# Optimization experiments

Measured on AMD Instinct MI355X. Metric: run time of the kernel, lower is better.

## Reference

```python
import jax, jax.numpy as jnp
import numpy as np

B, S, D = 2, 2048, 2048
H = 16
DR = 64      # qk_rope_head_dim
DN = 64      # qk_nope_head_dim
DQK = DN + DR
DV = 128     # v_head_dim
QLR = 1536   # q_lora_rank
KVLR = 1024  # kv_lora_rank
THETA = 10000.0


def setup_inputs() -> dict:
    key = jax.random.key(0)
    ks = jax.random.split(key, 8)
    init = lambda k, shape: (jax.random.normal(k, shape, jnp.float32) * 0.02)
    x = jax.random.normal(ks[0], (B, S, D), jnp.float32)
    wq_a = init(ks[1], (QLR, D))
    q_norm_w = jnp.ones((QLR,), jnp.float32)
    wq_b = init(ks[2], (H * DQK, QLR))
    wkv_a = init(ks[3], (KVLR + DR, D))
    kv_norm_w = jnp.ones((KVLR,), jnp.float32)
    wkv_b = init(ks[4], (H * (DN + DV), KVLR))
    wo = init(ks[5], (D, H * DV))
    # rotary frequencies: angle[t, i] = t / theta^(2i/DR)  (complex freqs_cis = cos + i sin)
    inv_freq = 1.0 / (THETA ** (jnp.arange(0, DR, 2, dtype=jnp.float32) / DR))
    ang = jnp.arange(S, dtype=jnp.float32)[:, None] * inv_freq[None, :]  # [S, DR/2]
    freqs_cos, freqs_sin = jnp.cos(ang), jnp.sin(ang)
    # causal additive mask (large negative instead of -inf for grad safety)
    mask = jnp.where(jnp.triu(jnp.ones((S, S), bool), 1), -1e9, 0.0).astype(jnp.float32)
    return dict(x=x, wq_a=wq_a, q_norm_w=q_norm_w, wq_b=wq_b, wkv_a=wkv_a,
                kv_norm_w=kv_norm_w, wkv_b=wkv_b, wo=wo, mask=mask,
                freqs_cos=freqs_cos, freqs_sin=freqs_sin, start_pos=0)


def _rmsnorm(x, w, eps=1e-6):
    return x * jax.lax.rsqrt(jnp.mean(x * x, axis=-1, keepdims=True) + eps) * w


def _rope(x, cos, sin):
    # x: [B, S, h, d]; complex multiply on interleaved (even, odd) pairs
    x0, x1 = x[..., ::2], x[..., 1::2]
    c = cos[None, :, None, :]
    s = sin[None, :, None, :]
    return jnp.stack([x0 * c - x1 * s, x0 * s + x1 * c], axis=-1).reshape(x.shape)


def reference(x, wq_a, q_norm_w, wq_b, wkv_a, kv_norm_w, wkv_b, wo,
              mask, freqs_cos, freqs_sin, start_pos):
    # start_pos == 0 prefill: KV cache[:end_pos] equals current K/V.
    scale = DQK ** -0.5
    # low-rank Q: wq_b(q_norm(wq_a(x)))
    q = _rmsnorm(x @ wq_a.T, q_norm_w) @ wq_b.T
    q = q.reshape(B, S, H, DQK)
    q_nope, q_pe = q[..., :DN], q[..., DN:]
    q_pe = _rope(q_pe, freqs_cos, freqs_sin)
    # latent KV
    kv = x @ wkv_a.T                              # [B, S, KVLR + DR]
    c_kv, k_pe = kv[..., :KVLR], kv[..., KVLR:]
    k_pe = _rope(k_pe[:, :, None, :], freqs_cos, freqs_sin)   # [B, S, 1, DR]
    kv2 = (_rmsnorm(c_kv, kv_norm_w) @ wkv_b.T).reshape(B, S, H, DN + DV)
    k_nope, v = kv2[..., :DN], kv2[..., DN:]
    k = jnp.concatenate([k_nope, jnp.broadcast_to(k_pe, (B, S, H, DR))], axis=-1)
    qf = jnp.concatenate([q_nope, q_pe], axis=-1)             # [B, S, H, DQK]
    # scores laid out [B, S(q), H, T(k)] as in the torch code
    scores = jnp.einsum('bshd,bthd->bsht', qf, k) * scale + mask[None, :, None, :]
    attn = jax.nn.softmax(scores.astype(jnp.float32), axis=-1).astype(x.dtype)
    out = jnp.einsum('bsht,bthd->bshd', attn, v)              # [B, S, H, DV]
    return out.reshape(B, S, H * DV) @ wo.T
```

## Files before the change

kernel.cpp:

```cpp
#include <hip/hip_runtime.h>
#include <hip/hip_bf16.h>


using bf16 = __hip_bfloat16;
typedef __attribute__((ext_vector_type(8))) short bf16x8;
typedef __attribute__((ext_vector_type(4))) float f32x4;

#define S_ 2048
#define NEG_BIG (-1e30f)
#define LOG2E 1.4426950408889634f

static __device__ __forceinline__ f32x4 mfma16(bf16x8 a, bf16x8 b, f32x4 c) {
    return __builtin_amdgcn_mfma_f32_16x16x32_bf16(a, b, c, 0, 0, 0);
}

static __device__ __forceinline__ void gload_lds16(const bf16* g, bf16* l) {
    __builtin_amdgcn_global_load_lds(
        (const __attribute__((address_space(1))) void*)g,
        (__attribute__((address_space(3))) void*)l, 16, 0, 0);
}

__global__ __launch_bounds__(256) void f2b(const float* __restrict__ src,
                                           bf16* __restrict__ dst, int n4) {
    int i = blockIdx.x * 256 + threadIdx.x;
    if (i < n4) {
        float4 v = ((const float4*)src)[i];
        alignas(8) bf16 t[4];
        t[0] = (bf16)v.x; t[1] = (bf16)v.y; t[2] = (bf16)v.z; t[3] = (bf16)v.w;
        ((uint2*)dst)[i] = *(const uint2*)t;
    }
}

template <bool C_F32>
__global__ __launch_bounds__(256) void gemm_bt(const bf16* __restrict__ A,
                                               const bf16* __restrict__ Bw,
                                               void* __restrict__ Cv,
                                               int M, int N, int K,
                                               int lda, int ldb, int ldc) {
    __shared__ bf16 As[2][128 * 32];
    __shared__ bf16 Bs[2][128 * 32];
    const int tid = threadIdx.x;
    const int m0 = blockIdx.x * 128;
    const int n0 = blockIdx.y * 128;
    const int w = tid >> 6, lane = tid & 63, quad = lane >> 4, l15 = lane & 15;
    const int wr = (w >> 1) * 64, wc = (w & 1) * 64;

    f32x4 acc[4][4];
#pragma unroll
    for (int i = 0; i < 4; i++)
#pragma unroll
        for (int j = 0; j < 4; j++) acc[i][j] = (f32x4){0.f, 0.f, 0.f, 0.f};

    auto stage = [&](int buf, int k0) {
#pragma unroll
        for (int cc = 0; cc < 2; cc++) {
            int c = tid + cc * 256;
            int row = c >> 2;
            int chunk = (c & 3) ^ ((row >> 1) & 3);
            gload_lds16(A + (size_t)(m0 + row) * lda + k0 + chunk * 8, &As[buf][c * 8]);
            gload_lds16(Bw + (size_t)(n0 + row) * ldb + k0 + chunk * 8, &Bs[buf][c * 8]);
        }
    };

    stage(0, 0);
    __syncthreads();
    int cur = 0;
    for (int k0 = 0; k0 < K; k0 += 32) {
        if (k0 + 32 < K) stage(cur ^ 1, k0 + 32);
        const bf16* Asc = As[cur];
        const bf16* Bsc = Bs[cur];
        bf16x8 af[4], bfr[4];
#pragma unroll
        for (int mi = 0; mi < 4; mi++) {
            int row = wr + mi * 16 + l15;
            int chunkE = quad ^ ((row >> 1) & 3);
            af[mi] = *(const bf16x8*)(&Asc[row * 32 + chunkE * 8]);
        }
#pragma unroll
        for (int ni = 0; ni < 4; ni++) {
            int row = wc + ni * 16 + l15;
            int chunkE = quad ^ ((row >> 1) & 3);
            bfr[ni] = *(const bf16x8*)(&Bsc[row * 32 + chunkE * 8]);
        }
#pragma unroll
        for (int mi = 0; mi < 4; mi++)
#pragma unroll
            for (int ni = 0; ni < 4; ni++)
                acc[mi][ni] = mfma16(af[mi], bfr[ni], acc[mi][ni]);
        __syncthreads();
        cur ^= 1;
    }

#pragma unroll
    for (int mi = 0; mi < 4; mi++) {
#pragma unroll
        for (int ni = 0; ni < 4; ni++) {
            int col = n0 + wc + ni * 16 + l15;
            if (col < N) {
#pragma unroll
                for (int r = 0; r < 4; r++) {
                    int row = m0 + wr + mi * 16 + quad * 4 + r;
                    if (C_F32) ((float*)Cv)[(size_t)row * ldc + col] = acc[mi][ni][r];
                    else       ((bf16*)Cv)[(size_t)row * ldc + col] = (bf16)acc[mi][ni][r];
                }
            }
        }
    }
}

__global__ void rmsnorm_ip(bf16* __restrict__ buf, const float* __restrict__ w,
                           int cols, int ld) {
    int row = blockIdx.x;
    bf16* p = buf + (size_t)row * ld;
    float ss = 0.f;
    for (int c = threadIdx.x; c < cols; c += 256) {
        float v = __bfloat162float(p[c]);
        ss += v * v;
    }
#pragma unroll
    for (int off = 32; off; off >>= 1) ss += __shfl_down(ss, off, 64);
    __shared__ float red[4];
    __shared__ float rnorm_s;
    if ((threadIdx.x & 63) == 0) red[threadIdx.x >> 6] = ss;
    __syncthreads();
    if (threadIdx.x == 0)
        rnorm_s = rsqrtf((red[0] + red[1] + red[2] + red[3]) / cols + 1e-6f);
    __syncthreads();
    float rn = rnorm_s;
    for (int c = threadIdx.x; c < cols; c += 256) {
        float v = __bfloat162float(p[c]);
        p[c] = (bf16)(v * rn * w[c]);
    }
}

__global__ void rope_k(const bf16* __restrict__ cq, bf16* __restrict__ kpe,
                       const float* __restrict__ fc, const float* __restrict__ fs) {
    int id = blockIdx.x * 256 + threadIdx.x;
    int row = id >> 5, i = id & 31;
    int s = row & (S_ - 1);
    const bf16* p = cq + (size_t)row * 2624 + 1024 + 2 * i;
    float x0 = __bfloat162float(p[0]), x1 = __bfloat162float(p[1]);
    float c = fc[s * 32 + i], sn = fs[s * 32 + i];
    bf16* q = kpe + (size_t)row * 64 + 2 * i;
    q[0] = (bf16)(x0 * c - x1 * sn);
    q[1] = (bf16)(x0 * sn + x1 * c);
}

__global__ void rope_q(bf16* __restrict__ qb, const float* __restrict__ fc,
                       const float* __restrict__ fs) {
    int id = blockIdx.x * 256 + threadIdx.x;
    int row = id >> 9, rest = id & 511, h = rest >> 5, i = rest & 31;
    int s = row & (S_ - 1);
    bf16* p = qb + (size_t)row * 2048 + h * 128 + 64 + 2 * i;
    float x0 = __bfloat162float(p[0]), x1 = __bfloat162float(p[1]);
    float c = fc[s * 32 + i], sn = fs[s * 32 + i];
    p[0] = (bf16)(x0 * c - x1 * sn);
    p[1] = (bf16)(x0 * sn + x1 * c);
}

__global__ __launch_bounds__(512) void attn_kernel(const bf16* __restrict__ Qg,
                                                   const bf16* __restrict__ KV2,
                                                   const bf16* __restrict__ KPE,
                                                   bf16* __restrict__ Og) {
    __shared__ bf16 Ks[64 * 128];
    __shared__ bf16 Vt[128 * 64];
    __shared__ bf16 Ps[8][16 * 64];
    const int tid = threadIdx.x;
    const int h = blockIdx.y;
    const int b = blockIdx.z;
    const int w = tid >> 6, lane = tid & 63, quad = lane >> 4, l15 = lane & 15;
    const int grp = w >> 2, wl = w & 3;
    const int jB = 31 - (int)blockIdx.x;
    const int q0 = (grp ? jB : (int)blockIdx.x) * 64;
    const int qrow = q0 + wl * 16 + l15;
    const float scl2 = 0.08838834764831845f * LOG2E;

    bf16x8 qf[4];
    {
        const bf16* qp = Qg + ((size_t)(b * S_) + qrow) * 2048 + h * 128 + quad * 8;
#pragma unroll
        for (int kk = 0; kk < 4; kk++) qf[kk] = *(const bf16x8*)(qp + kk * 32);
    }

    f32x4 acc_o[8];
#pragma unroll
    for (int j = 0; j < 8; j++) acc_o[j] = (f32x4){0.f, 0.f, 0.f, 0.f};
    float m_i = NEG_BIG, l_i = 0.f;
    const int s_base = q0 + wl * 16 + quad * 4;
    const int tend = jB * 64;

    const int dv0 = (tid >> 4) * 4;
    const int tv0 = (tid & 15) * 4;

    for (int t0 = 0; t0 <= tend; t0 += 64) {
        __syncthreads();
#pragma unroll
        for (int cc = 0; cc < 2; cc++) {
            int c = tid + cc * 512;
            int trow = c >> 4, chunk = c & 15;
            int col8 = chunk * 8;
            size_t grow = (size_t)(b * S_) + t0 + trow;
            int4 v;
            if (col8 < 64) v = *(const int4*)(KV2 + grow * 3072 + h * 192 + col8);
            else           v = *(const int4*)(KPE + grow * 64 + col8 - 64);
            int chunkE = chunk ^ (trow & 7);
            *(int4*)(&Ks[trow * 128 + chunkE * 8]) = v;
        }
        {
            size_t grow0 = (size_t)(b * S_) + t0 + tv0;
            alignas(16) bf16 va[4][4];
#pragma unroll
            for (int i = 0; i < 4; i++)
                *(uint2*)va[i] = *(const uint2*)(KV2 + (grow0 + i) * 3072 + h * 192 + 64 + dv0);
#pragma unroll
            for (int j = 0; j < 4; j++) {
                alignas(8) bf16 tmp[4] = {va[0][j], va[1][j], va[2][j], va[3][j]};
                int dv = dv0 + j;
                int cE = (tv0 >> 3) ^ (dv & 7);
                *(uint2*)(&Vt[dv * 64 + cE * 8 + (tv0 & 7)]) = *(uint2*)tmp;
            }
        }
        __syncthreads();
        if (t0 > q0) continue;

        f32x4 sc[4];
#pragma unroll
        for (int ni = 0; ni < 4; ni++) sc[ni] = (f32x4){0.f, 0.f, 0.f, 0.f};
#pragma unroll
        for (int kk = 0; kk < 4; kk++) {
#pragma unroll
            for (int ni = 0; ni < 4; ni++) {
                int trow = ni * 16 + l15;
                int chunkE = (kk * 4 + quad) ^ (trow & 7);
                bf16x8 kf = *(const bf16x8*)(&Ks[trow * 128 + chunkE * 8]);
                sc[ni] = mfma16(kf, qf[kk], sc[ni]);
            }
        }
        float xv[4][4];
        float pmax = NEG_BIG;
#pragma unroll
        for (int ni = 0; ni < 4; ni++) {
#pragma unroll
            for (int r = 0; r < 4; r++) {
                int t = t0 + ni * 16 + quad * 4 + r;
                float x = sc[ni][r] * scl2;
                if (t > qrow) x = NEG_BIG;
                xv[ni][r] = x;
                pmax = fmaxf(pmax, x);
            }
        }
        pmax = fmaxf(pmax, __shfl_xor(pmax, 16, 64));
        pmax = fmaxf(pmax, __shfl_xor(pmax, 32, 64));
        if (!__all(pmax - m_i <= 8.0f)) {
            float mn = fmaxf(m_i, pmax);
            float alpha = exp2f(m_i - mn);
            m_i = mn;
            l_i *= alpha;
            float ar[4];
#pragma unroll
            for (int r = 0; r < 4; r++) ar[r] = __shfl(alpha, quad * 4 + r, 64);
#pragma unroll
            for (int nj = 0; nj < 8; nj++)
#pragma unroll
                for (int r = 0; r < 4; r++) acc_o[nj][r] *= ar[r];
        }
        float rsum = 0.f;
#pragma unroll
        for (int ni = 0; ni < 4; ni++)
#pragma unroll
            for (int r = 0; r < 4; r++) {
                float e = exp2f(xv[ni][r] - m_i);
                xv[ni][r] = e;
                rsum += e;
            }
        rsum += __shfl_xor(rsum, 16, 64);
        rsum += __shfl_xor(rsum, 32, 64);
        l_i += rsum;

#pragma unroll
        for (int ni = 0; ni < 4; ni++) {
            int tb = ni * 16 + quad * 4;
            int cE = (tb >> 3) ^ (l15 & 7);
            alignas(8) bf16 tmp[4] = {(bf16)xv[ni][0], (bf16)xv[ni][1],
                                      (bf16)xv[ni][2], (bf16)xv[ni][3]};
            *(uint2*)(&Ps[w][l15 * 64 + cE * 8 + (tb & 7)]) = *(uint2*)tmp;
        }
#pragma unroll
        for (int kk2 = 0; kk2 < 2; kk2++) {
            int cEp = (kk2 * 4 + quad) ^ (l15 & 7);
            bf16x8 pf = *(const bf16x8*)(&Ps[w][l15 * 64 + cEp * 8]);
#pragma unroll
            for (int nj = 0; nj < 8; nj++) {
                int dv = nj * 16 + l15;
                int chunkE = (kk2 * 4 + quad) ^ (dv & 7);
                bf16x8 vf = *(const bf16x8*)(&Vt[dv * 64 + chunkE * 8]);
                acc_o[nj] = mfma16(pf, vf, acc_o[nj]);
            }
        }
    }
    float lr[4];
#pragma unroll
    for (int r = 0; r < 4; r++) lr[r] = __shfl(l_i, quad * 4 + r, 64);
#pragma unroll
    for (int nj = 0; nj < 8; nj++) {
        int col = h * 128 + nj * 16 + l15;
#pragma unroll
        for (int r = 0; r < 4; r++) {
            float v = acc_o[nj][r] / lr[r];
            Og[((size_t)(b * S_) + s_base + r) * 2048 + col] = (bf16)v;
        }
    }
}

extern "C" void kernel_launch(void* const* d_in, const int* in_sizes, int n_in,
                              void* d_out, int out_size, void* d_ws, size_t ws_size,
                              hipStream_t stream) {
    const float* x        = (const float*)d_in[0];
    const float* wq_a     = (const float*)d_in[1];
    const float* q_norm_w = (const float*)d_in[2];
    const float* wq_b     = (const float*)d_in[3];
    const float* wkv_a    = (const float*)d_in[4];
    const float* kv_norm_w= (const float*)d_in[5];
    const float* wkv_b    = (const float*)d_in[6];
    const float* wo       = (const float*)d_in[7];
    const float* fcos     = (const float*)d_in[9];
    const float* fsin     = (const float*)d_in[10];
    float* out = (float*)d_out;

    char* ws = (char*)d_ws;
    bf16* kv2   = (bf16*)(ws);
    bf16* kpe   = (bf16*)(ws + 25165824);
    bf16* cq    = (bf16*)(ws + 25690112);
    bf16* xb    = (bf16*)(ws + 47185920);
    bf16* wslot = (bf16*)(ws + 63963136);
    bf16* attno = cq;
    bf16* qbuf  = (bf16*)d_out;

    dim3 blk(256);
    f2b<<<8192, blk, 0, stream>>>(x, xb, 2097152);
    f2b<<<2176, blk, 0, stream>>>(wkv_a, wslot, 557056);
    f2b<<<3072, blk, 0, stream>>>(wq_a, wslot + 1088 * 2048, 786432);
    gemm_bt<false><<<dim3(32, 21), blk, 0, stream>>>(xb, wslot, cq, 4096, 2624, 2048, 2048, 2048, 2624);
    rope_k<<<512, blk, 0, stream>>>(cq, kpe, fcos, fsin);
    rmsnorm_ip<<<4096, blk, 0, stream>>>(cq, kv_norm_w, 1024, 2624);
    f2b<<<3072, blk, 0, stream>>>(wkv_b, wslot, 786432);
    gemm_bt<false><<<dim3(32, 24), blk, 0, stream>>>(cq, wslot, kv2, 4096, 3072, 1024, 2624, 1024, 3072);
    rmsnorm_ip<<<4096, blk, 0, stream>>>(cq + 1088, q_norm_w, 1536, 2624);
    f2b<<<3072, blk, 0, stream>>>(wq_b, wslot, 786432);
    gemm_bt<false><<<dim3(32, 16), blk, 0, stream>>>(cq + 1088, wslot, qbuf, 4096, 2048, 1536, 2624, 1536, 2048);
    rope_q<<<8192, blk, 0, stream>>>(qbuf, fcos, fsin);
    attn_kernel<<<dim3(16, 16, 2), dim3(512), 0, stream>>>(qbuf, kv2, kpe, attno);
    f2b<<<4096, blk, 0, stream>>>(wo, wslot, 1048576);
    gemm_bt<true><<<dim3(32, 16), blk, 0, stream>>>(attno, wslot, out, 4096, 2048, 2048, 2048, 2048, 2048);
}
```

Measured before the change: 477.4 us.

## Keep P in registers for PV MFMA and swizzle GEMM workgroup order

The attention kernel no longer writes the softmax probabilities to shared memory and reads them back. It packs them directly into the MFMA A-operand from registers and permutes the V operand reads to match the K-index ordering. The change removes an LDS round trip and the Ps buffer, at the cost of two 8-byte V loads per MFMA instead of one 16-byte load. Separately, the GEMM remaps workgroup IDs in groups of 8, which is aimed at L2/MALL locality across XCDs.

```diff
diff --git a/kernel.cpp b/kernel.cpp
--- a/kernel.cpp
+++ b/kernel.cpp
@@ -40,8 +40,18 @@
     __shared__ bf16 As[2][128 * 32];
     __shared__ bf16 Bs[2][128 * 32];
     const int tid = threadIdx.x;
-    const int m0 = blockIdx.x * 128;
-    const int n0 = blockIdx.y * 128;
+    int bx = blockIdx.x, by = blockIdx.y;
+    {
+        int nwg = gridDim.x * gridDim.y;
+        if ((nwg & 7) == 0) {
+            int wg = by * gridDim.x + bx;
+            int swz = (wg & 7) * (nwg >> 3) + (wg >> 3);
+            bx = swz % gridDim.x;
+            by = swz / gridDim.x;
+        }
+    }
+    const int m0 = bx * 128;
+    const int n0 = by * 128;
     const int w = tid >> 6, lane = tid & 63, quad = lane >> 4, l15 = lane & 15;
     const int wr = (w >> 1) * 64, wc = (w & 1) * 64;
 
@@ -164,7 +174,6 @@
                                                    bf16* __restrict__ Og) {
     __shared__ bf16 Ks[64 * 128];
     __shared__ bf16 Vt[128 * 64];
-    __shared__ bf16 Ps[8][16 * 64];
     const int tid = threadIdx.x;
     const int h = blockIdx.y;
     const int b = blockIdx.z;
@@ -278,22 +287,25 @@
         l_i += rsum;
 
 #pragma unroll
-        for (int ni = 0; ni < 4; ni++) {
-            int tb = ni * 16 + quad * 4;
-            int cE = (tb >> 3) ^ (l15 & 7);
-            alignas(8) bf16 tmp[4] = {(bf16)xv[ni][0], (bf16)xv[ni][1],
-                                      (bf16)xv[ni][2], (bf16)xv[ni][3]};
-            *(uint2*)(&Ps[w][l15 * 64 + cE * 8 + (tb & 7)]) = *(uint2*)tmp;
-        }
-#pragma unroll
-        for (int kk2 = 0; kk2 < 2; kk2++) {
-            int cEp = (kk2 * 4 + quad) ^ (l15 & 7);
-            bf16x8 pf = *(const bf16x8*)(&Ps[w][l15 * 64 + cEp * 8]);
+        for (int sg = 0; sg < 2; sg++) {
+            alignas(16) bf16 pfa[8];
+#pragma unroll
+            for (int j = 0; j < 4; j++) {
+                pfa[j]     = (bf16)xv[2 * sg][j];
+                pfa[j + 4] = (bf16)xv[2 * sg + 1][j];
+            }
+            bf16x8 pf = *(const bf16x8*)pfa;
+            const int cLo = sg * 4 + (quad >> 1);
+            const int cHi = cLo + 2;
+            const int off = (quad & 1) * 4;
 #pragma unroll
             for (int nj = 0; nj < 8; nj++) {
                 int dv = nj * 16 + l15;
-                int chunkE = (kk2 * 4 + quad) ^ (dv & 7);
-                bf16x8 vf = *(const bf16x8*)(&Vt[dv * 64 + chunkE * 8]);
+                int d7 = dv & 7;
+                alignas(16) bf16 vfa[8];
+                *(uint2*)&vfa[0] = *(const uint2*)&Vt[dv * 64 + ((cLo ^ d7) * 8) + off];
+                *(uint2*)&vfa[4] = *(const uint2*)&Vt[dv * 64 + ((cHi ^ d7) * 8) + off];
+                bf16x8 vf = *(const bf16x8*)vfa;
                 acc_o[nj] = mfma16(pf, vf, acc_o[nj]);
             }
         }
```

Result: no change. 482.0 us (+1.0%).
